# Performance work log

Measured on AMD Instinct MI355X. Metric: run time of the kernel, lower is better.

## Reference

```python
import jax, jax.numpy as jnp
import numpy as np

K = 4
TEMPERATURE = 34.0
IN_CH = 256
OUT_CH = 256
KSIZE = 3
PAD = 1
HIDDEN = int(2 * IN_CH * 0.25) + 1  # pool_mode='mix' doubles channels -> 129


def setup_inputs() -> dict:
    key = jax.random.key(0)
    ks = jax.random.split(key, 6)
    x = jax.random.normal(ks[0], (32, IN_CH, 56, 56), dtype=jnp.float32)
    # dynamic kernel bank [K, O, C, k, k]
    weight = jax.random.normal(ks[1], (K, OUT_CH, IN_CH, KSIZE, KSIZE), dtype=jnp.float32) * 0.05
    bias_k = jnp.zeros((K, OUT_CH), dtype=jnp.float32)
    # attention MLP (1x1 convs on pooled [B, 2C, 1, 1] == linear layers)
    w1 = jax.random.normal(ks[2], (HIDDEN, 2 * IN_CH), dtype=jnp.float32) * 0.06  # fc1, no bias
    w2 = jax.random.normal(ks[3], (K, HIDDEN), dtype=jnp.float32) * 0.12
    b2 = jnp.zeros((K,), dtype=jnp.float32)
    return {"x": x, "weight": weight, "bias_k": bias_k, "w1": w1, "w2": w2, "b2": b2}


def _attention(x, w1, w2, b2):
    # mix pooling: concat(avg, max) over spatial dims -> [B, 2C]
    avg = jnp.mean(x, axis=(2, 3))
    mx = jnp.max(x, axis=(2, 3))
    p = jnp.concatenate([avg, mx], axis=1)
    h = jax.nn.relu(jnp.einsum('bc,hc->bh', p, w1))
    logits = jnp.einsum('bh,kh->bk', h, w2) + b2
    return jax.nn.softmax(logits / TEMPERATURE, axis=1)  # [B, K]


def reference(x, weight, bias_k, w1, w2, b2):
    B, C, H, W = x.shape
    attn = _attention(x, w1, w2, b2)  # [B, K]
    # per-sample aggregated kernels [B, O, C, k, k]
    agg_w = jnp.einsum('bk,kocuv->bocuv', attn, weight)
    agg_b = attn @ bias_k  # [B, O]
    # grouped-conv trick: treat batch as groups
    xg = x.reshape(1, B * C, H, W)
    wg = agg_w.reshape(B * OUT_CH, C, KSIZE, KSIZE)
    out = jax.lax.conv_general_dilated(
        xg, wg,
        window_strides=(1, 1),
        padding=[(PAD, PAD), (PAD, PAD)],
        dimension_numbers=('NCHW', 'OIHW', 'NCHW'),
        feature_group_count=B,
    )  # [1, B*O, H, W]
    out = out.reshape(B, OUT_CH, H, W) + agg_b[:, :, None, None]
    return out
```

## Files before the change

### kernel.cpp

```cpp
#include <hip/hip_runtime.h>
#include <math.h>

#define BB 32
#define CC 256
#define OO 256
#define HW 56
#define SP (HW*HW)
#define KK 4
#define HID 129
#define TEMP 34.0f
#define PROW 58
#define PLANE (PROW*PROW*32)
#define PLANEB (PROW*PROW*64)
#define NSLOT 348
#define QSLOT 350
#define QSTRIDE (QSLOT*16)
#define NPIECE (4*QSLOT)
#define XA_B 8192
#define XB_B 24576

typedef unsigned short u16;
typedef unsigned int uint32;
typedef __attribute__((ext_vector_type(8))) short bf16x8;
typedef __attribute__((ext_vector_type(4))) float f32x4;

#define WAITVM(n) asm volatile("s_waitcnt vmcnt(" #n ")" ::: "memory")
#define WAITLGKM() asm volatile("s_waitcnt lgkmcnt(0)" ::: "memory")

__device__ __forceinline__ u16 f2bf(float f) {
    union { float f; uint32 u; } v; v.f = f;
    uint32 r = v.u + 0x7FFF + ((v.u >> 16) & 1);
    return (u16)(r >> 16);
}

__device__ __forceinline__ void gload16(const void* g, void* l) {
    __builtin_amdgcn_global_load_lds(
        (const __attribute__((address_space(1))) unsigned int*)g,
        (__attribute__((address_space(3))) unsigned int*)l, 16, 0, 0);
}

__global__ __launch_bounds__(256) void trans_pool(const float* __restrict__ x,
                                                  u16* __restrict__ xt,
                                                  float* __restrict__ pooled) {
    const int cb = blockIdx.x, b = blockIdx.y;
    const int tid = threadIdx.x;
    const int lane = tid & 63, wave = tid >> 6;
    const float* xp = x + ((size_t)b * CC + cb * 32) * SP;
    u16* xtb = xt + (size_t)(b * 8 + cb) * PLANE;

    if (tid < 228) {
        int slot;
        if (tid < 58)       slot = tid;
        else if (tid < 116) slot = 57 * 58 + (tid - 58);
        else if (tid < 172) slot = (tid - 116 + 1) * 58;
        else                slot = (tid - 172 + 1) * 58 + 57;
        bf16x8 z = {};
        #pragma unroll
        for (int j = 0; j < 4; ++j)
            *(bf16x8*)&xtb[(size_t)slot * 32 + j * 8] = z;
    }

    float psum[32], pmax[32];
    #pragma unroll
    for (int c = 0; c < 32; ++c) { psum[c] = 0.f; pmax[c] = -INFINITY; }

    for (int p0 = 0; p0 < SP; p0 += 256) {
        const int p = p0 + tid;
        const bool v = p < SP;
        const int pc = v ? p : (SP - 1);
        u16 ob[32];
        #pragma unroll
        for (int c = 0; c < 32; ++c) {
            const float vv = xp[(size_t)c * SP + pc];
            if (v) { psum[c] += vv; pmax[c] = fmaxf(pmax[c], vv); }
            ob[c] = f2bf(vv);
        }
        if (v) {
            const int slot = (p / 56 + 1) * 58 + (p % 56 + 1);
            #pragma unroll
            for (int j = 0; j < 4; ++j)
                *(bf16x8*)&xtb[(size_t)slot * 32 + j * 8] = *(bf16x8*)&ob[j * 8];
        }
    }
    #pragma unroll
    for (int c = 0; c < 32; ++c) {
        #pragma unroll
        for (int off = 32; off >= 1; off >>= 1) {
            psum[c] += __shfl_xor(psum[c], off, 64);
            pmax[c] = fmaxf(pmax[c], __shfl_xor(pmax[c], off, 64));
        }
    }
    __shared__ float ssum[4][32];
    __shared__ float smax[4][32];
    if (lane == 0) {
        #pragma unroll
        for (int c = 0; c < 32; ++c) { ssum[wave][c] = psum[c]; smax[wave][c] = pmax[c]; }
    }
    __syncthreads();
    if (tid < 32) {
        const float s = ssum[0][tid] + ssum[1][tid] + ssum[2][tid] + ssum[3][tid];
        const float m = fmaxf(fmaxf(smax[0][tid], smax[1][tid]),
                              fmaxf(smax[2][tid], smax[3][tid]));
        pooled[b * (2 * CC) + cb * 32 + tid]      = s / (float)SP;
        pooled[b * (2 * CC) + CC + cb * 32 + tid] = m;
    }
}

__global__ __launch_bounds__(256) void attn_kernel(const float* __restrict__ pooled,
                                                   const float* __restrict__ w1,
                                                   const float* __restrict__ w2,
                                                   const float* __restrict__ b2,
                                                   const float* __restrict__ bias_k,
                                                   float* __restrict__ attn,
                                                   float* __restrict__ agg_b) {
    const int b = blockIdx.x;
    const int tid = threadIdx.x;
    __shared__ float p[2 * CC];
    __shared__ float h[HID];
    __shared__ float a[KK];
    for (int i = tid; i < 2 * CC; i += 256) p[i] = pooled[b * 2 * CC + i];
    __syncthreads();
    if (tid < HID) {
        float s = 0.f;
        const float* w1r = w1 + (size_t)tid * (2 * CC);
        for (int c = 0; c < 2 * CC; ++c) s = fmaf(p[c], w1r[c], s);
        h[tid] = fmaxf(s, 0.f);
    }
    __syncthreads();
    if (tid == 0) {
        float lg[KK];
        float m = -INFINITY;
        for (int k = 0; k < KK; ++k) {
            float s = b2[k];
            for (int i = 0; i < HID; ++i) s = fmaf(h[i], w2[k * HID + i], s);
            lg[k] = s / TEMP;
            m = fmaxf(m, lg[k]);
        }
        float den = 0.f;
        for (int k = 0; k < KK; ++k) { lg[k] = expf(lg[k] - m); den += lg[k]; }
        for (int k = 0; k < KK; ++k) { a[k] = lg[k] / den; attn[b * KK + k] = a[k]; }
    }
    __syncthreads();
    if (tid < OO) {
        float s = 0.f;
        #pragma unroll
        for (int k = 0; k < KK; ++k) s = fmaf(a[k], bias_k[k * OO + tid], s);
        agg_b[b * OO + tid] = s;
    }
}

__global__ __launch_bounds__(512) void agg_kernel(const float* __restrict__ weight,
                                                  const float* __restrict__ attn,
                                                  u16* __restrict__ wT2) {
    const int bx = blockIdx.x;
    const int oy = bx & 1, cb = (bx >> 1) & 7, osub = bx >> 4;
    const int tid = threadIdx.x;
    const int oloc = tid >> 5, cl_ = tid & 31;
    const int o = oy * 128 + osub * 16 + oloc;
    const int c = cb * 32 + cl_;
    const int kg = cl_ >> 3, cl = cl_ & 7;

    __shared__ float at[BB * KK];
    __shared__ u16 tbuf[4][9][4][128];

    if (tid < BB * KK) at[tid] = attn[tid];

    float w[KK][9];
    #pragma unroll
    for (int k = 0; k < KK; ++k) {
        const float* wp = weight + (size_t)((k * OO + o) * CC + c) * 9;
        #pragma unroll
        for (int uv = 0; uv < 9; ++uv) w[k][uv] = wp[uv];
    }

    int pbb[9]; size_t goff[9]; int loff[9];
    #pragma unroll
    for (int i = 0; i < 9; ++i) {
        const int p = i * 512 + tid;
        const int bb = p / 1152, q = p % 1152;
        const int uv = q >> 7, pkg = (q >> 5) & 3, dq = q & 31;
        pbb[i] = bb;
        goff[i] = (size_t)(uv * 16 + cb * 2 + oy) * 4096 + pkg * 1024 + osub * 128 + dq * 4;
        loff[i] = ((bb * 9 + uv) * 4 + pkg) * 128 + dq * 4;
    }
    __syncthreads();

    for (int br = 0; br < 8; ++br) {
        #pragma unroll
        for (int bb = 0; bb < 4; ++bb) {
            const int b = br * 4 + bb;
            const float a0 = at[b*KK+0], a1 = at[b*KK+1], a2 = at[b*KK+2], a3 = at[b*KK+3];
            #pragma unroll
            for (int uv = 0; uv < 9; ++uv) {
                const float s = a0*w[0][uv] + a1*w[1][uv] + a2*w[2][uv] + a3*w[3][uv];
                tbuf[bb][uv][kg][oloc * 8 + cl] = f2bf(s);
            }
        }
        __syncthreads();
        #pragma unroll
        for (int i = 0; i < 9; ++i) {
            const int b = br * 4 + pbb[i];
            *(uint2*)(wT2 + (size_t)b * 144 * 4096 + goff[i]) =
                *(const uint2*)((const u16*)tbuf + loff[i]);
        }
        __syncthreads();
    }
}

__global__ __launch_bounds__(512, 4) void conv_mfma(const u16* __restrict__ xt,
                                                    const u16* __restrict__ wT2,
                                                    const float* __restrict__ agg_b,
                                                    float* __restrict__ out) {
    const int id   = blockIdx.x;
    const int g    = id >> 3;
    const int b    = (id & 7) + 8 * (g / 28);
    const int tile = g % 28;
    const int px   = tile % 14, oy = tile / 14;
    const int tid  = threadIdx.x;
    const int lane = tid & 63, wave = tid >> 6;
    const int wm = wave & 3, wn = wave >> 2;
    const int l15 = lane & 15, kg = lane >> 4;
    const int p0 = px * 224;

    __shared__ char XA[3][XA_B];
    __shared__ char XB[2][XB_B];

    uint32 soff[3];
    #pragma unroll
    for (int k = 0; k < 3; ++k) {
        int i = k * 512 + tid;
        if (i >= NPIECE) i = NPIECE - 1;
        const int q = i / QSLOT, slot = i % QSLOT;
        soff[k] = (uint32)((px * 232 + slot) * 64 + q * 16);
    }

    int bboff[7];
    #pragma unroll
    for (int nf = 0; nf < 7; ++nf) {
        const int n = wn * 112 + nf * 16 + l15;
        const int S = (n / 56 + 1) * 58 + (n % 56 + 1);
        bboff[nf] = kg * QSTRIDE + S * 16;
    }

    const int aoff0 = kg * 2048 + (wm * 32 + l15) * 16;
    const int aoff1 = aoff0 + 16 * 16;

    const char* xgb = (const char*)xt + (size_t)(b * 8) * PLANEB;
    const char* wAb = (const char*)wT2 + (size_t)b * 9 * 8 * 2 * 8192
                     + (size_t)oy * 8192;
    const size_t tb = (size_t)tid * 16;

    f32x4 acc[2][7];
    #pragma unroll
    for (int mf = 0; mf < 2; ++mf)
        #pragma unroll
        for (int nf = 0; nf < 7; ++nf)
            acc[mf][nf] = (f32x4)0.f;

    #pragma unroll
    for (int k = 0; k < 3; ++k)
        gload16(xgb + soff[k], &XB[0][k * 8192 + wave * 1024]);
    gload16(wAb + (size_t)(0 * 8 + 0) * 2 * 8192 + tb, &XA[0][wave * 1024]);
    gload16(wAb + (size_t)(1 * 8 + 0) * 2 * 8192 + tb, &XA[1][wave * 1024]);

    for (int cb = 0; cb < 8; ++cb) {
        const char* RB = XB[cb & 1];
        char* WB = XB[(cb & 1) ^ 1];
        const char* xg_next = xgb + (size_t)((cb + 1) & 7) * PLANEB;

        #pragma unroll
        for (int uv = 0; uv < 9; ++uv) {
            if (uv == 2 || uv == 3) WAITVM(3);
            else if (uv == 1 || uv == 4) WAITVM(2);
            else WAITVM(1);
            __builtin_amdgcn_s_barrier();

            const char* RA = XA[uv % 3];
            bf16x8 av0 = *(const bf16x8*)(RA + aoff0);
            bf16x8 av1 = *(const bf16x8*)(RA + aoff1);
            const int dby = ((uv / 3 - 1) * 58 + (uv % 3 - 1)) * 16;
            bf16x8 bv[7];
            #pragma unroll
            for (int nf = 0; nf < 7; ++nf)
                bv[nf] = *(const bf16x8*)(RB + bboff[nf] + dby);

            {
                const int uv_s = (uv + 2 < 9) ? uv + 2 : uv - 7;
                const int cb_s = (uv + 2 < 9) ? cb : ((cb + 1) & 7);
                gload16(wAb + (size_t)(uv_s * 8 + cb_s) * 2 * 8192 + tb,
                        &XA[(uv + 2) % 3][wave * 1024]);
            }
            if (uv < 3)
                gload16(xg_next + soff[uv], &WB[uv * 8192 + wave * 1024]);

            WAITLGKM();
            __builtin_amdgcn_sched_barrier(0);
            __builtin_amdgcn_s_setprio(1);
            #pragma unroll
            for (int nf = 0; nf < 7; ++nf) {
                acc[0][nf] = __builtin_amdgcn_mfma_f32_16x16x32_bf16(av0, bv[nf], acc[0][nf], 0, 0, 0);
                acc[1][nf] = __builtin_amdgcn_mfma_f32_16x16x32_bf16(av1, bv[nf], acc[1][nf], 0, 0, 0);
            }
            __builtin_amdgcn_s_setprio(0);
        }
    }

    const int obase = oy * 128 + wm * 32;
    float* outb = out + (size_t)b * OO * SP;
    #pragma unroll
    for (int mf = 0; mf < 2; ++mf) {
        #pragma unroll
        for (int r = 0; r < 4; ++r) {
            const int o = obase + mf * 16 + kg * 4 + r;
            const float bias = agg_b[b * OO + o];
            #pragma unroll
            for (int nf = 0; nf < 7; ++nf) {
                const int p = p0 + wn * 112 + nf * 16 + l15;
                outb[(size_t)o * SP + p] = acc[mf][nf][r] + bias;
            }
        }
    }
}

extern "C" void kernel_launch(void* const* d_in, const int* in_sizes, int n_in,
                              void* d_out, int out_size, void* d_ws, size_t ws_size,
                              hipStream_t stream) {
    const float* x      = (const float*)d_in[0];
    const float* weight = (const float*)d_in[1];
    const float* bias_k = (const float*)d_in[2];
    const float* w1     = (const float*)d_in[3];
    const float* w2     = (const float*)d_in[4];
    const float* b2     = (const float*)d_in[5];
    float* out = (float*)d_out;

    u16* x_t = (u16*)d_ws;
    u16* wT2 = x_t + (size_t)BB * 8 * PLANE;
    float* ws_f   = (float*)(wT2 + (size_t)BB * 9 * OO * CC);
    float* pooled = ws_f;
    float* attn   = ws_f + BB * 2 * CC;
    float* agg_b  = attn + BB * KK;

    trans_pool<<<dim3(8, BB), 256, 0, stream>>>(x, x_t, pooled);
    attn_kernel<<<BB, 256, 0, stream>>>(pooled, w1, w2, b2, bias_k, attn, agg_b);
    agg_kernel<<<128, 512, 0, stream>>>(weight, attn, wT2);
    conv_mfma<<<896, 512, 0, stream>>>(x_t, wT2, agg_b, out);
}
```

Before: 193.0 us.

## Halve conv block to 4 waves with 64x112 per-wave MFMA tiles

The conv kernel now runs 256 threads (4 waves) per block instead of 512. Each wave covers 64 output channels by 112 pixels (4x7 MFMA fragments) rather than 32x112, so each B fragment read from LDS is reused across more MFMAs. Global-to-LDS staging is split into more 16-byte loads per thread, and the vmcnt waits are retuned to match. The larger accumulator tile raises register pressure and leaves fewer waves per CU to hide latency, with launch bounds relaxed to (256,2).

```diff
diff --git a/kernel.cpp b/kernel.cpp
--- a/kernel.cpp
+++ b/kernel.cpp
@@ -207,7 +207,7 @@
     }
 }
 
-__global__ __launch_bounds__(512, 4) void conv_mfma(const u16* __restrict__ xt,
+__global__ __launch_bounds__(256, 2) void conv_mfma(const u16* __restrict__ xt,
                                                     const u16* __restrict__ wT2,
                                                     const float* __restrict__ agg_b,
                                                     float* __restrict__ out) {
@@ -218,17 +218,17 @@
     const int px   = tile % 14, oy = tile / 14;
     const int tid  = threadIdx.x;
     const int lane = tid & 63, wave = tid >> 6;
-    const int wm = wave & 3, wn = wave >> 2;
+    const int wm = wave & 1, wn = wave >> 1;
     const int l15 = lane & 15, kg = lane >> 4;
     const int p0 = px * 224;
 
     __shared__ char XA[3][XA_B];
     __shared__ char XB[2][XB_B];
 
-    uint32 soff[3];
-    #pragma unroll
-    for (int k = 0; k < 3; ++k) {
-        int i = k * 512 + tid;
+    uint32 soff[6];
+    #pragma unroll
+    for (int k = 0; k < 6; ++k) {
+        int i = k * 256 + tid;
         if (i >= NPIECE) i = NPIECE - 1;
         const int q = i / QSLOT, slot = i % QSLOT;
         soff[k] = (uint32)((px * 232 + slot) * 64 + q * 16);
@@ -242,26 +242,34 @@
         bboff[nf] = kg * QSTRIDE + S * 16;
     }
 
-    const int aoff0 = kg * 2048 + (wm * 32 + l15) * 16;
-    const int aoff1 = aoff0 + 16 * 16;
+    int aoff[4];
+    #pragma unroll
+    for (int mf = 0; mf < 4; ++mf)
+        aoff[mf] = kg * 2048 + (wm * 64 + mf * 16 + l15) * 16;
 
     const char* xgb = (const char*)xt + (size_t)(b * 8) * PLANEB;
     const char* wAb = (const char*)wT2 + (size_t)b * 9 * 8 * 2 * 8192
                      + (size_t)oy * 8192;
     const size_t tb = (size_t)tid * 16;
 
-    f32x4 acc[2][7];
-    #pragma unroll
-    for (int mf = 0; mf < 2; ++mf)
+    f32x4 acc[4][7];
+    #pragma unroll
+    for (int mf = 0; mf < 4; ++mf)
         #pragma unroll
         for (int nf = 0; nf < 7; ++nf)
             acc[mf][nf] = (f32x4)0.f;
 
     #pragma unroll
-    for (int k = 0; k < 3; ++k)
-        gload16(xgb + soff[k], &XB[0][k * 8192 + wave * 1024]);
-    gload16(wAb + (size_t)(0 * 8 + 0) * 2 * 8192 + tb, &XA[0][wave * 1024]);
-    gload16(wAb + (size_t)(1 * 8 + 0) * 2 * 8192 + tb, &XA[1][wave * 1024]);
+    for (int k = 0; k < 6; ++k)
+        gload16(xgb + soff[k], &XB[0][k * 4096 + wave * 1024]);
+    {
+        const char* a0 = wAb;
+        gload16(a0 + tb,        &XA[0][wave * 1024]);
+        gload16(a0 + 4096 + tb, &XA[0][4096 + wave * 1024]);
+        const char* a1 = wAb + (size_t)(1 * 8 + 0) * 2 * 8192;
+        gload16(a1 + tb,        &XA[1][wave * 1024]);
+        gload16(a1 + 4096 + tb, &XA[1][4096 + wave * 1024]);
+    }
 
     for (int cb = 0; cb < 8; ++cb) {
         const char* RB = XB[cb & 1];
@@ -270,14 +278,16 @@
 
         #pragma unroll
         for (int uv = 0; uv < 9; ++uv) {
-            if (uv == 2 || uv == 3) WAITVM(3);
-            else if (uv == 1 || uv == 4) WAITVM(2);
-            else WAITVM(1);
+            if (uv == 1 || uv == 6) WAITVM(3);
+            else if (uv >= 2 && uv <= 5) WAITVM(4);
+            else WAITVM(2);
             __builtin_amdgcn_s_barrier();
 
             const char* RA = XA[uv % 3];
-            bf16x8 av0 = *(const bf16x8*)(RA + aoff0);
-            bf16x8 av1 = *(const bf16x8*)(RA + aoff1);
+            bf16x8 av[4];
+            #pragma unroll
+            for (int mf = 0; mf < 4; ++mf)
+                av[mf] = *(const bf16x8*)(RA + aoff[mf]);
             const int dby = ((uv / 3 - 1) * 58 + (uv % 3 - 1)) * 16;
             bf16x8 bv[7];
             #pragma unroll
@@ -287,28 +297,31 @@
             {
                 const int uv_s = (uv + 2 < 9) ? uv + 2 : uv - 7;
                 const int cb_s = (uv + 2 < 9) ? cb : ((cb + 1) & 7);
-                gload16(wAb + (size_t)(uv_s * 8 + cb_s) * 2 * 8192 + tb,
-                        &XA[(uv + 2) % 3][wave * 1024]);
+                const char* src = wAb + (size_t)(uv_s * 8 + cb_s) * 2 * 8192;
+                char* dst = &XA[(uv + 2) % 3][0];
+                gload16(src + tb,        dst + wave * 1024);
+                gload16(src + 4096 + tb, dst + 4096 + wave * 1024);
             }
-            if (uv < 3)
-                gload16(xg_next + soff[uv], &WB[uv * 8192 + wave * 1024]);
+            if (uv < 6)
+                gload16(xg_next + soff[uv], &WB[uv * 4096 + wave * 1024]);
 
             WAITLGKM();
             __builtin_amdgcn_sched_barrier(0);
             __builtin_amdgcn_s_setprio(1);
             #pragma unroll
             for (int nf = 0; nf < 7; ++nf) {
-                acc[0][nf] = __builtin_amdgcn_mfma_f32_16x16x32_bf16(av0, bv[nf], acc[0][nf], 0, 0, 0);
-                acc[1][nf] = __builtin_amdgcn_mfma_f32_16x16x32_bf16(av1, bv[nf], acc[1][nf], 0, 0, 0);
+                #pragma unroll
+                for (int mf = 0; mf < 4; ++mf)
+                    acc[mf][nf] = __builtin_amdgcn_mfma_f32_16x16x32_bf16(av[mf], bv[nf], acc[mf][nf], 0, 0, 0);
             }
             __builtin_amdgcn_s_setprio(0);
         }
     }
 
-    const int obase = oy * 128 + wm * 32;
+    const int obase = oy * 128 + wm * 64;
     float* outb = out + (size_t)b * OO * SP;
     #pragma unroll
-    for (int mf = 0; mf < 2; ++mf) {
+    for (int mf = 0; mf < 4; ++mf) {
         #pragma unroll
         for (int r = 0; r < 4; ++r) {
             const int o = obase + mf * 16 + kg * 4 + r;
@@ -343,5 +356,5 @@
     trans_pool<<<dim3(8, BB), 256, 0, stream>>>(x, x_t, pooled);
     attn_kernel<<<BB, 256, 0, stream>>>(pooled, w1, w2, b2, bias_k, attn, agg_b);
     agg_kernel<<<128, 512, 0, stream>>>(weight, attn, wT2);
-    conv_mfma<<<896, 512, 0, stream>>>(x_t, wT2, agg_b, out);
-}
+    conv_mfma<<<896, 256, 0, stream>>>(x_t, wT2, agg_b, out);
+}
```

After: 189.3 us, median of 2. No clear change (-1.9%).
